# Performance work log

Hardware: AMD Instinct MI355X
Metric: run time of the kernel (lower is better)

The kernel has to match this reference:

```python
import jax, jax.numpy as jnp
import numpy as np

EPS_IN = 1e-5   # InstanceNorm eps
EPS_L1 = 1e-12  # F.normalize eps


def conv1x1(x, w, b):
    # x: [B,C,H,W], w: [O,C], b: [O]
    return jnp.einsum('bchw,oc->bohw', x, w) + b[None, :, None, None]


def conv3x3_reflect(x, w, b):
    xp = jnp.pad(x, ((0, 0), (0, 0), (1, 1), (1, 1)), mode='reflect')
    y = jax.lax.conv_general_dilated(xp, w, (1, 1), 'VALID',
                                     dimension_numbers=('NCHW', 'OIHW', 'NCHW'))
    return y + b[None, :, None, None]


def instance_norm(x):
    mu = x.mean(axis=(2, 3), keepdims=True)
    var = x.var(axis=(2, 3), keepdims=True)  # biased, matches torch InstanceNorm
    return (x - mu) * jax.lax.rsqrt(var + EPS_IN)


def res_block(x, w1, b1, w2, b2):
    h = jax.nn.relu(instance_norm(conv3x3_reflect(x, w1, b1)))
    h = instance_norm(conv3x3_reflect(h, w2, b2))
    return x + h


def _nearest_idx(out_size, in_size):
    # torch F.interpolate(mode='nearest'): src = floor(dst * in/out)
    return (np.arange(out_size) * in_size) // out_size


def forward(x, mask, g_w, g_b, theta_w, theta_b, phi_w, phi_b, W_w, W_b,
            res_w1, res_b1, res_w2, res_b2):
    B, C, H, Wd = x.shape
    N = H * Wd
    g_x = conv1x1(x, g_w, g_b).reshape(B, -1, N).transpose(0, 2, 1)      # [B,N,Ci]
    theta_x = conv1x1(x, theta_w, theta_b).reshape(B, -1, N).transpose(0, 2, 1)
    phi_x = conv1x1(x, phi_w, phi_b).reshape(B, -1, N)                   # [B,Ci,N]
    f = jnp.einsum('bnc,bcm->bnm', theta_x, phi_x)  # temperature = 1.0
    f_div_C = jax.nn.softmax(f, axis=2)
    # mask pipeline
    m = jax.image.resize(mask, (B, 1, H, Wd), method='linear')  # bilinear, half-pixel (align_corners=False)
    m = jnp.where(m > 0, 1.0, m)
    m = 1.0 - m
    hi = _nearest_idx(H, mask.shape[2])
    wi = _nearest_idx(Wd, mask.shape[3])
    tmp = (1.0 - mask)[:, :, hi][:, :, :, wi]  # nearest upsample of (1-mask)
    m = m * tmp                                 # [B,1,H,W]
    f_div_C = f_div_C * m.reshape(B, 1, N)      # broadcast instead of N^2 repeat
    # re_norm=True: L1 renormalize along keys
    f_div_C = f_div_C / jnp.maximum(jnp.sum(jnp.abs(f_div_C), axis=2, keepdims=True), EPS_L1)
    y = jnp.einsum('bnm,bmc->bnc', f_div_C, g_x)             # [B,N,Ci]
    y = y.transpose(0, 2, 1).reshape(B, -1, H, Wd)
    W_y = conv1x1(y, W_w, W_b)
    for i in range(3):
        W_y = res_block(W_y, res_w1[i], res_b1[i], res_w2[i], res_b2[i])
    z = m * x + (1.0 - m) * W_y
    return z


def setup_inputs() -> dict:
    key = jax.random.key(0)
    ks = jax.random.split(key, 16)
    B, C, H, W = 4, 256, 64, 64
    x = jax.random.normal(ks[0], (B, C, H, W), dtype=jnp.float32)
    mask = (jax.random.uniform(ks[1], (B, 1, 32, 32)) < 0.5).astype(jnp.float32)
    s = 0.02
    d = {
        'x': x, 'mask': mask,
        'g_w': jax.random.normal(ks[2], (C, C), jnp.float32) * s,
        'g_b': jnp.zeros((C,), jnp.float32),
        'theta_w': jax.random.normal(ks[3], (C, C), jnp.float32) * s,
        'theta_b': jnp.zeros((C,), jnp.float32),
        'phi_w': jax.random.normal(ks[4], (C, C), jnp.float32) * s,
        'phi_b': jnp.zeros((C,), jnp.float32),
        'W_w': jax.random.normal(ks[5], (C, C), jnp.float32) * s,
        'W_b': jnp.zeros((C,), jnp.float32),
        'res_w1': jax.random.normal(ks[6], (3, C, C, 3, 3), jnp.float32) * s,
        'res_b1': jnp.zeros((3, C), jnp.float32),
        'res_w2': jax.random.normal(ks[7], (3, C, C, 3, 3), jnp.float32) * s,
        'res_b2': jnp.zeros((3, C), jnp.float32),
    }
    return d


def reference(x, mask, g_w, g_b, theta_w, theta_b, phi_w, phi_b, W_w, W_b,
              res_w1, res_b1, res_w2, res_b2):
    return forward(x, mask, g_w, g_b, theta_w, theta_b, phi_w, phi_b, W_w, W_b,
                   res_w1, res_b1, res_w2, res_b2)
```

## Files before the change

kernel.cpp:

```cpp
#include <hip/hip_runtime.h>

#define BB   4
#define CC   256
#define NPIX 4096
#define PB   1048576
#define NTOT 16384

typedef __attribute__((ext_vector_type(8))) short bf16x8;
typedef __attribute__((ext_vector_type(4))) float f32x4;
typedef __attribute__((ext_vector_type(4))) unsigned short u16x4;

__device__ __forceinline__ unsigned short f2b(float f) {
  union { float f; unsigned u; } v; v.f = f;
  unsigned r = v.u + 0x7fffu + ((v.u >> 16) & 1u);
  return (unsigned short)(r >> 16);
}
__device__ __forceinline__ float b2f(unsigned short h) {
  union { unsigned u; float f; } v; v.u = ((unsigned)h) << 16;
  return v.f;
}
__device__ __forceinline__ f32x4 mfma16(bf16x8 a, bf16x8 b, f32x4 c) {
  return __builtin_amdgcn_mfma_f32_16x16x32_bf16(a, b, c, 0, 0, 0);
}
__device__ __forceinline__ void gload_lds16(const unsigned short* g, unsigned short* l) {
  __builtin_amdgcn_global_load_lds(
      (const __attribute__((address_space(1))) unsigned int*)g,
      (__attribute__((address_space(3))) unsigned int*)l, 16, 0, 0);
}
__device__ __forceinline__ int remap_px(int n, int dh, int dw) {
  int h = (n >> 6) + dh;
  int w = (n & 63) + dw;
  h = h < 0 ? 1 : (h > 63 ? 62 : h);
  w = w < 0 ? 1 : (w > 63 ? 62 : w);
  return (h << 6) | w;
}

__global__ void repack_w1x1_k(const float* __restrict__ tw, const float* __restrict__ pw,
                              const float* __restrict__ gw, const float* __restrict__ Ww,
                              unsigned short* __restrict__ dst) {
  int i = blockIdx.x * 256 + threadIdx.x;
  dst[i]           = f2b(tw[i]);
  dst[65536 + i]   = f2b(pw[i]);
  dst[131072 + i]  = f2b(gw[i]);
  dst[196608 + i]  = f2b(Ww[i]);
}

__global__ void repack_bias_k(const float* __restrict__ tb, const float* __restrict__ pb,
                              const float* __restrict__ gb, const float* __restrict__ Wb,
                              float* __restrict__ bias) {
  int i = blockIdx.x * 256 + threadIdx.x;
  float v;
  if (i < 256) v = tb[i];
  else if (i < 512) v = pb[i - 256];
  else if (i < 768) v = gb[i - 512];
  else v = Wb[i - 768];
  bias[i] = v;
}

__global__ void repack_res_k(const float* __restrict__ w1, const float* __restrict__ w2,
                             unsigned short* __restrict__ wk) {
  int idx = blockIdx.x * 256 + threadIdx.x;
  if (idx >= 1769472) return;
  int t = idx % 9;
  int rest = idx / 9;
  int c = rest & 255;
  int o = (rest >> 8) & 255;
  int i = rest >> 16;
  size_t d = (size_t)t * 65536 + o * 256 + c;
  wk[(size_t)(2 * i)     * 589824 + d] = f2b(w1[idx]);
  wk[(size_t)(2 * i + 1) * 589824 + d] = f2b(w2[idx]);
}

__global__ void prep_mask_k(const float* __restrict__ mask, float* __restrict__ m) {
  int idx = blockIdx.x * 256 + threadIdx.x;
  if (idx >= BB * NPIX) return;
  int b = idx >> 12, n = idx & 4095;
  int h = n >> 6, w = n & 63;
  const float* M = mask + b * 1024;
  float sh = 0.5f * h - 0.25f, sw = 0.5f * w - 0.25f;
  int h0 = (int)floorf(sh), w0 = (int)floorf(sw);
  float th = sh - h0, tw = sw - w0;
  int h0c = min(max(h0, 0), 31), h1c = min(max(h0 + 1, 0), 31);
  int w0c = min(max(w0, 0), 31), w1c = min(max(w0 + 1, 0), 31);
  float v = (1.f - th) * ((1.f - tw) * M[h0c * 32 + w0c] + tw * M[h0c * 32 + w1c])
          +        th  * ((1.f - tw) * M[h1c * 32 + w0c] + tw * M[h1c * 32 + w1c]);
  float inv = v > 0.f ? 0.f : 1.f;
  float tmp = 1.f - M[(h >> 1) * 32 + (w >> 1)];
  m[idx] = inv * tmp;
}

__global__ void mask_scan_k(const float* __restrict__ mbuf, int* __restrict__ ci,
                            int* __restrict__ kcount) {
  int b = blockIdx.x;
  int tid = threadIdx.x;
  __shared__ int sc[256];
  const float* mb = mbuf + b * 4096;
  int n0 = tid * 16, cnt = 0;
  float mv[16];
  #pragma unroll
  for (int i = 0; i < 16; ++i) { mv[i] = mb[n0 + i]; cnt += mv[i] > 0.f ? 1 : 0; }
  sc[tid] = cnt;
  __syncthreads();
  for (int off = 1; off < 256; off <<= 1) {
    int v = sc[tid];
    int u = tid >= off ? sc[tid - off] : 0;
    __syncthreads();
    sc[tid] = v + u;
    __syncthreads();
  }
  int base = sc[tid] - cnt;
  int* cib = ci + b * 4096;
  #pragma unroll
  for (int i = 0; i < 16; ++i)
    if (mv[i] > 0.f) cib[base++] = n0 + i;
  if (tid == 255) kcount[b] = sc[255];
}

__global__ void gather_phi_k(const unsigned short* __restrict__ phb, const int* __restrict__ ci,
                             const int* __restrict__ kcount, unsigned short* __restrict__ phic) {
  int b = blockIdx.y;
  int Kb = kcount[b];
  int pad = (Kb + 63) & ~63;
  int j = blockIdx.x * 8 + (threadIdx.x >> 5);
  int cl = threadIdx.x & 31;
  if (j >= pad) return;
  bf16x8 v;
  if (j < Kb) {
    v = *(const bf16x8*)(phb + (size_t)b * PB + (size_t)ci[b * 4096 + j] * 256 + cl * 8);
  } else {
    for (int t = 0; t < 8; ++t) v[t] = 0;
  }
  *(bf16x8*)(phic + (size_t)b * PB + (size_t)j * 256 + cl * 8) = v;
}

__global__ void gather_g_k(const unsigned short* __restrict__ gbuf, const int* __restrict__ ci,
                           const int* __restrict__ kcount, unsigned short* __restrict__ gc) {
  int b = blockIdx.z;
  int Kb = kcount[b];
  int pad = (Kb + 63) & ~63;
  int c = blockIdx.y;
  int j = blockIdx.x * 256 + threadIdx.x;
  if (j >= pad) return;
  unsigned short v = 0;
  if (j < Kb) v = gbuf[(size_t)c * NTOT + b * 4096 + ci[b * 4096 + j]];
  gc[(size_t)c * NTOT + b * 4096 + j] = v;
}

__global__ void transpose_x_k(const float* __restrict__ x, unsigned short* __restrict__ xT) {
  __shared__ float T[64][65];
  int b = blockIdx.z;
  int n0 = blockIdx.x * 64, c0 = blockIdx.y * 64;
  int tx = threadIdx.x, ty = threadIdx.y;
  const float* xb = x + (size_t)b * PB;
  #pragma unroll
  for (int i = 0; i < 16; ++i) {
    int cl = ty + i * 4;
    T[cl][tx] = xb[(size_t)(c0 + cl) * NPIX + n0 + tx];
  }
  __syncthreads();
  unsigned short* ob = xT + (size_t)b * PB;
  #pragma unroll
  for (int i = 0; i < 16; ++i) {
    int nl = ty + i * 4;
    ob[(size_t)(n0 + nl) * CC + c0 + tx] = f2b(T[tx][nl]);
  }
}

template <int EPI, int TAPS>
__launch_bounds__(128, 2)
__global__ void gemm_w(const unsigned short* __restrict__ A,
                       const unsigned short* __restrict__ Bact,
                       const float* __restrict__ bias,
                       float* __restrict__ outF,
                       unsigned short* __restrict__ o0,
                       unsigned short* __restrict__ o1,
                       unsigned short* __restrict__ o2) {
  int m0 = blockIdx.y * 128;
  int bxs = (blockIdx.x & 7) * 32 + (blockIdx.x >> 3);
  int n0 = bxs * 64;
  int tid = threadIdx.x, lane = tid & 63, wid = tid >> 6;
  int r16 = lane & 15, g4 = lane >> 4;
  __shared__ __align__(16) unsigned short As[2 * 8192];
  __shared__ __align__(16) unsigned short Bs[2 * 4096];
  f32x4 acc[4][4] = {};
  int sr[8], sc[8];
  #pragma unroll
  for (int q = 0; q < 8; ++q) {
    sr[q] = (tid >> 3) + q * 16;
    sc[q] = (((tid * 16) & 127) ^ ((sr[q] & 7) << 4)) >> 1;
  }
  int q7 = r16 & 7;
  int ra[4], rbv[4];
  #pragma unroll
  for (int i = 0; i < 4; ++i) ra[i] = (wid * 64 + i * 16 + r16) * 128;
  #pragma unroll
  for (int j = 0; j < 4; ++j) rbv[j] = (j * 16 + r16) * 128;

  const int nsteps = TAPS * 4;

#define STAGE(st_, bs_) do {                                                      \
    int tap_ = (st_) >> 2, k0_ = ((st_) & 3) * 64;                                \
    const unsigned short* At_ = A + tap_ * 65536;                                 \
    _Pragma("unroll")                                                             \
    for (int q = 0; q < 8; ++q)                                                   \
      gload_lds16(At_ + (size_t)(m0 + sr[q]) * 256 + k0_ + sc[q],                 \
                  &As[(bs_) * 8192 + tid * 8 + q * 1024]);                        \
    _Pragma("unroll")                                                             \
    for (int q = 0; q < 4; ++q) {                                                 \
      int n_ = n0 + sr[q];                                                        \
      int bsrc_ = n_;                                                             \
      if (TAPS == 9) bsrc_ = (n_ & ~4095) | remap_px(n_ & 4095, tap_ / 3 - 1, tap_ % 3 - 1); \
      gload_lds16(Bact + (size_t)bsrc_ * 256 + k0_ + sc[q],                       \
                  &Bs[(bs_) * 4096 + tid * 8 + q * 1024]);                        \
    }                                                                             \
  } while (0)

#define COMPUTE(bs_) do {                                                         \
    _Pragma("unroll")                                                             \
    for (int kk = 0; kk < 2; ++kk) {                                              \
      bf16x8 af_[4], bf_[4];                                                      \
      _Pragma("unroll")                                                           \
      for (int i = 0; i < 4; ++i)                                                 \
        af_[i] = *(const bf16x8*)((const char*)As + (bs_) * 16384 + ra[i] +       \
                                  (((kk * 4 + g4) ^ q7) << 4));                   \
      _Pragma("unroll")                                                           \
      for (int j = 0; j < 4; ++j)                                                 \
        bf_[j] = *(const bf16x8*)((const char*)Bs + (bs_) * 8192 + rbv[j] +       \
                                  (((kk * 4 + g4) ^ q7) << 4));                   \
      _Pragma("unroll")                                                           \
      for (int i = 0; i < 4; ++i)                                                 \
        _Pragma("unroll")                                                         \
        for (int j = 0; j < 4; ++j)                                               \
          acc[i][j] = mfma16(af_[i], bf_[j], acc[i][j]);                          \
    }                                                                             \
  } while (0)

  STAGE(0, 0);
  for (int st = 0; st < nsteps; ++st) {
    __syncthreads();
    if (st + 1 < nsteps) STAGE(st + 1, (st + 1) & 1);
    COMPUTE(st & 1);
  }
#undef STAGE
#undef COMPUTE

  #pragma unroll
  for (int i = 0; i < 4; ++i) {
    int row = m0 + wid * 64 + i * 16 + g4 * 4;
    #pragma unroll
    for (int j = 0; j < 4; ++j) {
      int n = n0 + j * 16 + r16;
      f32x4 v = acc[i][j];
      if constexpr (EPI == 0) {
        int sec = row >> 8;
        int ch = row & 255;
        if (sec < 2) {
          u16x4 pk;
          #pragma unroll
          for (int r = 0; r < 4; ++r) pk[r] = f2b(v[r] + bias[row + r]);
          *(u16x4*)((sec ? o1 : o0) + (size_t)n * 256 + ch) = pk;
        } else {
          #pragma unroll
          for (int r = 0; r < 4; ++r)
            o2[(size_t)(ch + r) * NTOT + n] = f2b(v[r] + bias[row + r]);
        }
      } else if constexpr (EPI == 1) {
        u16x4 pk;
        #pragma unroll
        for (int r = 0; r < 4; ++r) pk[r] = f2b(v[r]);
        *(u16x4*)(o0 + (size_t)n * 256 + row) = pk;
      } else {
        #pragma unroll
        for (int r = 0; r < 4; ++r) v[r] += bias[row + r];
        *(f32x4*)(outF + (size_t)n * 256 + row) = v;
        u16x4 pk;
        #pragma unroll
        for (int r = 0; r < 4; ++r) pk[r] = f2b(v[r]);
        *(u16x4*)(o0 + (size_t)n * 256 + row) = pk;
      }
    }
  }
}

__launch_bounds__(512, 2)
__global__ void attn_k(const unsigned short* __restrict__ theta,
                       const unsigned short* __restrict__ phic,
                       const unsigned short* __restrict__ gc,
                       const int* __restrict__ kcount,
                       float* __restrict__ Op0,
                       float* __restrict__ Op1,
                       float2* __restrict__ ml2) {
  int f = blockIdx.x;
  int b = (f & 7) >> 1;
  int s = f & 1;
  int q0 = (f >> 3) * 128;
  int tid = threadIdx.x, lane = tid & 63, wid = tid >> 6;
  int r16 = lane & 15, g4 = lane >> 4;
  const unsigned short* th = theta + (size_t)b * PB;
  const unsigned short* phb = phic + (size_t)b * PB;

  int Kb = kcount[b];
  int nt = (Kb + 63) >> 6;
  int h = (nt + 1) >> 1;
  int t0 = s * h, t1 = min(nt, t0 + h);

  __shared__ __align__(16) unsigned short Kt[2][16384];
  __shared__ __align__(16) unsigned short Vt[2][16384];
  __shared__ __align__(16) unsigned short Plds[8][16][72];

  int qrow = q0 + wid * 16 + r16;
  bf16x8 aq[8];
  #pragma unroll
  for (int ks = 0; ks < 8; ++ks)
    aq[ks] = *(const bf16x8*)(th + (size_t)qrow * CC + ks * 32 + 8 * g4);

  f32x4 O[16];
  #pragma unroll
  for (int cf = 0; cf < 16; ++cf) { O[cf][0] = 0.f; O[cf][1] = 0.f; O[cf][2] = 0.f; O[cf][3] = 0.f; }
  float mrow[4] = {-1e30f, -1e30f, -1e30f, -1e30f};
  float lrow[4] = {0.f, 0.f, 0.f, 0.f};

  bf16x8 kst[4], vst[4];
  if (t0 < t1) {
    int k0g = t0 * 64;
    #pragma unroll
    for (int i = 0; i < 4; ++i) {
      int slot = wid * 4 + i;
      kst[i] = *(const bf16x8*)(phb + (size_t)(k0g + lane) * CC + slot * 8);
      vst[i] = *(const bf16x8*)(gc + (size_t)(i * 64 + lane) * NTOT + b * 4096 + k0g + wid * 8);
    }
    #pragma unroll
    for (int i = 0; i < 4; ++i) {
      int slot = wid * 4 + i;
      *(bf16x8*)&Kt[0][slot * 512 + lane * 8] = kst[i];
      *(bf16x8*)&Vt[0][wid * 2048 + i * 512 + lane * 8] = vst[i];
    }
  }
  __syncthreads();

  #pragma unroll 1
  for (int t = t0; t < t1; ++t) {
    int p = (t - t0) & 1;
    if (t + 1 < t1) {
      int k0g = (t + 1) * 64;
      #pragma unroll
      for (int i = 0; i < 4; ++i) {
        int slot = wid * 4 + i;
        kst[i] = *(const bf16x8*)(phb + (size_t)(k0g + lane) * CC + slot * 8);
        vst[i] = *(const bf16x8*)(gc + (size_t)(i * 64 + lane) * NTOT + b * 4096 + k0g + wid * 8);
      }
    }
    f32x4 S[4];
    #pragma unroll
    for (int ff = 0; ff < 4; ++ff) { S[ff][0] = 0.f; S[ff][1] = 0.f; S[ff][2] = 0.f; S[ff][3] = 0.f; }
    #pragma unroll
    for (int ks = 0; ks < 8; ++ks) {
      #pragma unroll
      for (int ff = 0; ff < 4; ++ff) {
        bf16x8 bk = *(const bf16x8*)&Kt[p][(ks * 4 + g4) * 512 + (ff * 16 + r16) * 8];
        S[ff] = mfma16(aq[ks], bk, S[ff]);
      }
    }
    bool mk[4];
    #pragma unroll
    for (int ff = 0; ff < 4; ++ff) mk[ff] = (t * 64 + ff * 16 + r16) < Kb;
    float scr[4];
    #pragma unroll
    for (int r = 0; r < 4; ++r) {
      float v = -1e30f;
      #pragma unroll
      for (int ff = 0; ff < 4; ++ff) v = fmaxf(v, mk[ff] ? S[ff][r] : -1e30f);
      v = fmaxf(v, __shfl_xor(v, 1));
      v = fmaxf(v, __shfl_xor(v, 2));
      v = fmaxf(v, __shfl_xor(v, 4));
      v = fmaxf(v, __shfl_xor(v, 8));
      float nm = fmaxf(mrow[r], v);
      scr[r] = __expf(mrow[r] - nm);
      mrow[r] = nm;
      lrow[r] *= scr[r];
    }
    float ps[4][4];
    float rsum[4] = {0.f, 0.f, 0.f, 0.f};
    #pragma unroll
    for (int ff = 0; ff < 4; ++ff)
      #pragma unroll
      for (int r = 0; r < 4; ++r) {
        float pp = mk[ff] ? __expf(S[ff][r] - mrow[r]) : 0.f;
        ps[ff][r] = pp;
        rsum[r] += pp;
      }
    #pragma unroll
    for (int r = 0; r < 4; ++r) {
      float sm = rsum[r];
      sm += __shfl_xor(sm, 1);
      sm += __shfl_xor(sm, 2);
      sm += __shfl_xor(sm, 4);
      sm += __shfl_xor(sm, 8);
      lrow[r] += sm;
    }
    #pragma unroll
    for (int cf = 0; cf < 16; ++cf) {
      O[cf][0] *= scr[0]; O[cf][1] *= scr[1]; O[cf][2] *= scr[2]; O[cf][3] *= scr[3];
    }
    #pragma unroll
    for (int ff = 0; ff < 4; ++ff)
      #pragma unroll
      for (int r = 0; r < 4; ++r)
        Plds[wid][g4 * 4 + r][ff * 16 + r16] = f2b(ps[ff][r]);
    #pragma unroll
    for (int ks2 = 0; ks2 < 2; ++ks2) {
      bf16x8 ap = *(const bf16x8*)&Plds[wid][r16][ks2 * 32 + 8 * g4];
      #pragma unroll
      for (int cf = 0; cf < 16; ++cf) {
        bf16x8 bv = *(const bf16x8*)&Vt[p][(ks2 * 4 + g4) * 2048 + (cf * 16 + r16) * 8];
        O[cf] = mfma16(ap, bv, O[cf]);
      }
    }
    if (t + 1 < t1) {
      #pragma unroll
      for (int i = 0; i < 4; ++i) {
        int slot = wid * 4 + i;
        *(bf16x8*)&Kt[p ^ 1][slot * 512 + lane * 8] = kst[i];
        *(bf16x8*)&Vt[p ^ 1][wid * 2048 + i * 512 + lane * 8] = vst[i];
      }
    }
    __syncthreads();
  }

  float* Opb = (s ? Op1 : Op0) + (size_t)b * NPIX * CC;
  #pragma unroll
  for (int cf = 0; cf < 16; ++cf)
    #pragma unroll
    for (int r = 0; r < 4; ++r)
      Opb[(size_t)(q0 + wid * 16 + g4 * 4 + r) * CC + cf * 16 + r16] = O[cf][r];
  if (r16 == 0) {
    #pragma unroll
    for (int r = 0; r < 4; ++r)
      ml2[(size_t)(s * BB + b) * NPIX + q0 + wid * 16 + g4 * 4 + r] =
          make_float2(mrow[r], lrow[r]);
  }
}

__global__ void attn_combine_k(const float* __restrict__ Op0, const float* __restrict__ Op1,
                               const float2* __restrict__ ml2, unsigned short* __restrict__ y) {
  size_t e = ((size_t)blockIdx.x * 256 + threadIdx.x) * 8;
  int bn = (int)(e >> 8);
  float2 a = ml2[bn];
  float2 c = ml2[16384 + bn];
  float M = fmaxf(a.x, c.x);
  float e0 = __expf(a.x - M), e1 = __expf(c.x - M);
  float L = a.y * e0 + c.y * e1;
  float sc = L > 1e-30f ? 1.f / L : 0.f;
  e0 *= sc; e1 *= sc;
  f32x4 p0 = *(const f32x4*)&Op0[e];
  f32x4 p1 = *(const f32x4*)&Op0[e + 4];
  f32x4 q0 = *(const f32x4*)&Op1[e];
  f32x4 q1 = *(const f32x4*)&Op1[e + 4];
  bf16x8 r;
  #pragma unroll
  for (int j = 0; j < 4; ++j) {
    r[j]     = (short)f2b(p0[j] * e0 + q0[j] * e1);
    r[4 + j] = (short)f2b(p1[j] * e0 + q1[j] * e1);
  }
  *(bf16x8*)&y[e] = r;
}

__global__ void in_stats_k(const unsigned short* __restrict__ v,
                           float* __restrict__ psum, float* __restrict__ psumsq) {
  int p = blockIdx.x;
  int b = blockIdx.y;
  int tid = threadIdx.x;
  int cg = (tid & 31) * 8;
  int rsub = tid >> 5;
  const unsigned short* base = v + (size_t)b * PB + (size_t)p * 128 * CC;
  float s[8] = {}, s2[8] = {};
  for (int it = 0; it < 16; ++it) {
    int row = rsub + it * 8;
    bf16x8 x = *(const bf16x8*)(base + (size_t)row * CC + cg);
    #pragma unroll
    for (int j = 0; j < 8; ++j) {
      float f = b2f((unsigned short)x[j]);
      s[j] += f; s2[j] += f * f;
    }
  }
  __shared__ float redS[8][256];
  __shared__ float redQ[8][256];
  #pragma unroll
  for (int j = 0; j < 8; ++j) { redS[rsub][cg + j] = s[j]; redQ[rsub][cg + j] = s2[j]; }
  __syncthreads();
  float a = 0.f, q = 0.f;
  #pragma unroll
  for (int r = 0; r < 8; ++r) { a += redS[r][tid]; q += redQ[r][tid]; }
  int o = (p * BB + b) * CC + tid;
  psum[o] = a; psumsq[o] = q;
}

__global__ void in_finalize_k(const float* __restrict__ psum, const float* __restrict__ psumsq,
                              float* __restrict__ mu, float* __restrict__ rs) {
  int bc = blockIdx.x * 256 + threadIdx.x;
  int b = bc >> 8, c = bc & 255;
  float s = 0.f, s2 = 0.f;
  for (int p = 0; p < 32; ++p) {
    s  += psum[(p * BB + b) * CC + c];
    s2 += psumsq[(p * BB + b) * CC + c];
  }
  float m_ = s * (1.f / 4096.f);
  float var = s2 * (1.f / 4096.f) - m_ * m_;
  var = var > 0.f ? var : 0.f;
  mu[bc] = m_;
  rs[bc] = rsqrtf(var + 1e-5f);
}

__global__ void normrelu_k(const unsigned short* __restrict__ src,
                           const float* __restrict__ mu, const float* __restrict__ rs,
                           unsigned short* __restrict__ dst) {
  size_t idx = (size_t)blockIdx.x * 256 + threadIdx.x;
  size_t e = idx * 8;
  if (e >= (size_t)BB * PB) return;
  int c = (int)(e & 255);
  int b = (int)(e >> 20);
  const float* mup = mu + b * 256 + c;
  const float* rsp = rs + b * 256 + c;
  bf16x8 v = *(const bf16x8*)(src + e);
  bf16x8 ov;
  #pragma unroll
  for (int j = 0; j < 8; ++j) {
    float f = (b2f((unsigned short)v[j]) - mup[j]) * rsp[j];
    ov[j] = (short)f2b(f > 0.f ? f : 0.f);
  }
  *(bf16x8*)(dst + e) = ov;
}

__global__ void resupdate_k(const unsigned short* __restrict__ c2,
                            const float* __restrict__ mu, const float* __restrict__ rs,
                            float* __restrict__ r, unsigned short* __restrict__ rb) {
  size_t idx = (size_t)blockIdx.x * 256 + threadIdx.x;
  size_t e = idx * 8;
  if (e >= (size_t)BB * PB) return;
  int c = (int)(e & 255);
  int b = (int)(e >> 20);
  const float* mup = mu + b * 256 + c;
  const float* rsp = rs + b * 256 + c;
  bf16x8 v = *(const bf16x8*)(c2 + e);
  bf16x8 ov;
  #pragma unroll
  for (int j = 0; j < 8; ++j) {
    float f = r[e + j] + (b2f((unsigned short)v[j]) - mup[j]) * rsp[j];
    r[e + j] = f;
    ov[j] = (short)f2b(f);
  }
  *(bf16x8*)(rb + e) = ov;
}

__global__ void final_blend_k(const float* __restrict__ x, const float* __restrict__ r,
                              const float* __restrict__ m, float* __restrict__ out) {
  __shared__ float T[64][65];
  int b = blockIdx.z;
  int n0 = blockIdx.x * 64, c0 = blockIdx.y * 64;
  int tx = threadIdx.x, ty = threadIdx.y;
  #pragma unroll
  for (int i = 0; i < 16; ++i) {
    int nl = ty + i * 4;
    T[nl][tx] = r[(size_t)b * PB + (size_t)(n0 + nl) * CC + c0 + tx];
  }
  __syncthreads();
  #pragma unroll
  for (int i = 0; i < 16; ++i) {
    int cl = ty + i * 4;
    int cg = c0 + cl, ng = n0 + tx;
    float mv = m[b * NPIX + ng];
    float xv = x[(size_t)b * PB + (size_t)cg * NPIX + ng];
    out[(size_t)b * PB + (size_t)cg * NPIX + ng] = mv * xv + (1.f - mv) * T[tx][cl];
  }
}

#define OFF_M    0UL
#define OFF_XT   65536UL
#define OFF_TH   8454144UL
#define OFF_PH   16842752UL
#define OFF_G    25231360UL
#define OFF_R    33619968UL
#define OFF_W1   50397184UL
#define OFF_WK   50921472UL
#define OFF_MU   57999360UL
#define OFF_RS   58003456UL
#define OFF_PS   58007552UL
#define OFF_PS2  58138624UL
#define OFF_OP1  58269696UL
#define OFF_ML   75046912UL
#define OFF_CI   75309056UL
#define OFF_KC   75374592UL
#define OFF_BIAS 75374848UL

extern "C" void kernel_launch(void* const* d_in, const int* in_sizes, int n_in,
                              void* d_out, int out_size, void* d_ws, size_t ws_size,
                              hipStream_t stream) {
  const float* x       = (const float*)d_in[0];
  const float* maskp   = (const float*)d_in[1];
  const float* g_w     = (const float*)d_in[2];
  const float* g_b     = (const float*)d_in[3];
  const float* theta_w = (const float*)d_in[4];
  const float* theta_b = (const float*)d_in[5];
  const float* phi_w   = (const float*)d_in[6];
  const float* phi_b   = (const float*)d_in[7];
  const float* W_w     = (const float*)d_in[8];
  const float* W_b     = (const float*)d_in[9];
  const float* res_w1  = (const float*)d_in[10];
  const float* res_w2  = (const float*)d_in[12];
  float* out = (float*)d_out;
  char* ws = (char*)d_ws;

  float*          mbuf = (float*)(ws + OFF_M);
  unsigned short* xT   = (unsigned short*)(ws + OFF_XT);
  unsigned short* phic = (unsigned short*)(ws + OFF_XT);
  unsigned short* ybuf = (unsigned short*)(ws + OFF_XT);
  unsigned short* thb  = (unsigned short*)(ws + OFF_TH);
  unsigned short* cbuf = (unsigned short*)(ws + OFF_TH);
  unsigned short* phb  = (unsigned short*)(ws + OFF_PH);
  unsigned short* gc   = (unsigned short*)(ws + OFF_PH);
  unsigned short* hbuf = (unsigned short*)(ws + OFF_PH);
  unsigned short* gbuf = (unsigned short*)(ws + OFF_G);
  unsigned short* rb   = (unsigned short*)(ws + OFF_G);
  float*          rbuf = (float*)(ws + OFF_R);
  float*          op0  = (float*)(ws + OFF_R);
  float*          op1  = (float*)(ws + OFF_OP1);
  float2*         ml2  = (float2*)(ws + OFF_ML);
  int*            ci   = (int*)(ws + OFF_CI);
  int*            kc   = (int*)(ws + OFF_KC);
  float*          biasS= (float*)(ws + OFF_BIAS);
  unsigned short* thw  = (unsigned short*)(ws + OFF_W1);
  unsigned short* Www  = (unsigned short*)(ws + OFF_W1 + 393216);
  unsigned short* wkres= (unsigned short*)(ws + OFF_WK);
  float*          mu   = (float*)(ws + OFF_MU);
  float*          rs   = (float*)(ws + OFF_RS);
  float*          psum = (float*)(ws + OFF_PS);
  float*          psq  = (float*)(ws + OFF_PS2);

  repack_w1x1_k<<<256, 256, 0, stream>>>(theta_w, phi_w, g_w, W_w, thw);
  repack_res_k<<<6912, 256, 0, stream>>>(res_w1, res_w2, wkres);
  repack_bias_k<<<4, 256, 0, stream>>>(theta_b, phi_b, g_b, W_b, biasS);
  prep_mask_k<<<64, 256, 0, stream>>>(maskp, mbuf);
  transpose_x_k<<<dim3(64, 4, 4), dim3(64, 4), 0, stream>>>(x, xT);

  gemm_w<0, 1><<<dim3(256, 6), 128, 0, stream>>>(thw, xT, biasS, nullptr, thb, phb, gbuf);

  mask_scan_k<<<4, 256, 0, stream>>>(mbuf, ci, kc);
  gather_phi_k<<<dim3(512, 4), 256, 0, stream>>>(phb, ci, kc, phic);
  gather_g_k<<<dim3(16, 256, 4), 256, 0, stream>>>(gbuf, ci, kc, gc);

  attn_k<<<256, 512, 0, stream>>>(thb, phic, gc, kc, op0, op1, ml2);
  attn_combine_k<<<2048, 256, 0, stream>>>(op0, op1, ml2, ybuf);

  gemm_w<2, 1><<<dim3(256, 2), 128, 0, stream>>>(Www, ybuf, biasS + 768, rbuf, rb, nullptr, nullptr);

  for (int i = 0; i < 3; ++i) {
    gemm_w<1, 9><<<dim3(256, 2), 128, 0, stream>>>(
        wkres + (size_t)(2 * i) * 589824, rb, nullptr, nullptr, cbuf, nullptr, nullptr);
    in_stats_k<<<dim3(32, 4), 256, 0, stream>>>(cbuf, psum, psq);
    in_finalize_k<<<4, 256, 0, stream>>>(psum, psq, mu, rs);
    normrelu_k<<<2048, 256, 0, stream>>>(cbuf, mu, rs, hbuf);
    gemm_w<1, 9><<<dim3(256, 2), 128, 0, stream>>>(
        wkres + (size_t)(2 * i + 1) * 589824, hbuf, nullptr, nullptr, cbuf, nullptr, nullptr);
    in_stats_k<<<dim3(32, 4), 256, 0, stream>>>(cbuf, psum, psq);
    in_finalize_k<<<4, 256, 0, stream>>>(psum, psq, mu, rs);
    resupdate_k<<<2048, 256, 0, stream>>>(cbuf, mu, rs, rbuf, rb);
  }

  final_blend_k<<<dim3(64, 4, 4), dim3(64, 4), 0, stream>>>(x, rbuf, mbuf, out);
}
```

Before: 589.6 us.

## Enlarge GEMM tiles to 128x128 and split-K the 3x3 convs with fused stats combine

New measurement: 499.8 us. 1.18x faster.

```diff
diff --git a/kernel.cpp b/kernel.cpp
--- a/kernel.cpp
+++ b/kernel.cpp
@@ -166,8 +166,8 @@
   }
 }
 
-template <int EPI, int TAPS>
-__launch_bounds__(128, 2)
+template <int EPI, int TAPS, int KSPLIT>
+__launch_bounds__(256, 2)
 __global__ void gemm_w(const unsigned short* __restrict__ A,
                        const unsigned short* __restrict__ Bact,
                        const float* __restrict__ bias,
@@ -176,42 +176,42 @@
                        unsigned short* __restrict__ o1,
                        unsigned short* __restrict__ o2) {
   int m0 = blockIdx.y * 128;
-  int bxs = (blockIdx.x & 7) * 32 + (blockIdx.x >> 3);
-  int n0 = bxs * 64;
+  int bxs = (blockIdx.x & 7) * 16 + (blockIdx.x >> 3);
+  int n0 = bxs * 128;
   int tid = threadIdx.x, lane = tid & 63, wid = tid >> 6;
+  int wm = wid >> 1, wn = wid & 1;
   int r16 = lane & 15, g4 = lane >> 4;
   __shared__ __align__(16) unsigned short As[2 * 8192];
-  __shared__ __align__(16) unsigned short Bs[2 * 4096];
+  __shared__ __align__(16) unsigned short Bs[2 * 8192];
   f32x4 acc[4][4] = {};
-  int sr[8], sc[8];
-  #pragma unroll
-  for (int q = 0; q < 8; ++q) {
-    sr[q] = (tid >> 3) + q * 16;
-    sc[q] = (((tid * 16) & 127) ^ ((sr[q] & 7) << 4)) >> 1;
-  }
+  int r0 = tid >> 3;
+  int scol = ((((tid * 16) & 127) ^ ((r0 & 7) << 4)) >> 1);
   int q7 = r16 & 7;
   int ra[4], rbv[4];
   #pragma unroll
-  for (int i = 0; i < 4; ++i) ra[i] = (wid * 64 + i * 16 + r16) * 128;
-  #pragma unroll
-  for (int j = 0; j < 4; ++j) rbv[j] = (j * 16 + r16) * 128;
+  for (int i = 0; i < 4; ++i) ra[i] = (wm * 64 + i * 16 + r16) * 128;
+  #pragma unroll
+  for (int j = 0; j < 4; ++j) rbv[j] = (wn * 64 + j * 16 + r16) * 128;
 
   const int nsteps = TAPS * 4;
+  const int span = nsteps / KSPLIT;
+  const int s0 = (KSPLIT > 1 ? blockIdx.z : 0) * span;
+  const int s1 = s0 + span;
 
 #define STAGE(st_, bs_) do {                                                      \
     int tap_ = (st_) >> 2, k0_ = ((st_) & 3) * 64;                                \
     const unsigned short* At_ = A + tap_ * 65536;                                 \
     _Pragma("unroll")                                                             \
-    for (int q = 0; q < 8; ++q)                                                   \
-      gload_lds16(At_ + (size_t)(m0 + sr[q]) * 256 + k0_ + sc[q],                 \
-                  &As[(bs_) * 8192 + tid * 8 + q * 1024]);                        \
+    for (int q = 0; q < 4; ++q)                                                   \
+      gload_lds16(At_ + (size_t)(m0 + r0 + q * 32) * 256 + k0_ + scol,            \
+                  &As[(bs_) * 8192 + tid * 8 + q * 2048]);                        \
     _Pragma("unroll")                                                             \
     for (int q = 0; q < 4; ++q) {                                                 \
-      int n_ = n0 + sr[q];                                                        \
+      int n_ = n0 + r0 + q * 32;                                                  \
       int bsrc_ = n_;                                                             \
       if (TAPS == 9) bsrc_ = (n_ & ~4095) | remap_px(n_ & 4095, tap_ / 3 - 1, tap_ % 3 - 1); \
-      gload_lds16(Bact + (size_t)bsrc_ * 256 + k0_ + sc[q],                       \
-                  &Bs[(bs_) * 4096 + tid * 8 + q * 1024]);                        \
+      gload_lds16(Bact + (size_t)bsrc_ * 256 + k0_ + scol,                        \
+                  &Bs[(bs_) * 8192 + tid * 8 + q * 2048]);                        \
     }                                                                             \
   } while (0)
 
@@ -225,7 +225,7 @@
                                   (((kk * 4 + g4) ^ q7) << 4));                   \
       _Pragma("unroll")                                                           \
       for (int j = 0; j < 4; ++j)                                                 \
-        bf_[j] = *(const bf16x8*)((const char*)Bs + (bs_) * 8192 + rbv[j] +       \
+        bf_[j] = *(const bf16x8*)((const char*)Bs + (bs_) * 16384 + rbv[j] +      \
                                   (((kk * 4 + g4) ^ q7) << 4));                   \
       _Pragma("unroll")                                                           \
       for (int i = 0; i < 4; ++i)                                                 \
@@ -235,21 +235,21 @@
     }                                                                             \
   } while (0)
 
-  STAGE(0, 0);
-  for (int st = 0; st < nsteps; ++st) {
+  STAGE(s0, 0);
+  for (int st = s0; st < s1; ++st) {
     __syncthreads();
-    if (st + 1 < nsteps) STAGE(st + 1, (st + 1) & 1);
-    COMPUTE(st & 1);
+    if (st + 1 < s1) STAGE(st + 1, (st + 1 - s0) & 1);
+    COMPUTE((st - s0) & 1);
   }
 #undef STAGE
 #undef COMPUTE
 
   #pragma unroll
   for (int i = 0; i < 4; ++i) {
-    int row = m0 + wid * 64 + i * 16 + g4 * 4;
+    int row = m0 + wm * 64 + i * 16 + g4 * 4;
     #pragma unroll
     for (int j = 0; j < 4; ++j) {
-      int n = n0 + j * 16 + r16;
+      int n = n0 + wn * 64 + j * 16 + r16;
       f32x4 v = acc[i][j];
       if constexpr (EPI == 0) {
         int sec = row >> 8;
@@ -269,7 +269,7 @@
         #pragma unroll
         for (int r = 0; r < 4; ++r) pk[r] = f2b(v[r]);
         *(u16x4*)(o0 + (size_t)n * 256 + row) = pk;
-      } else {
+      } else if constexpr (EPI == 2) {
         #pragma unroll
         for (int r = 0; r < 4; ++r) v[r] += bias[row + r];
         *(f32x4*)(outF + (size_t)n * 256 + row) = v;
@@ -277,9 +277,54 @@
         #pragma unroll
         for (int r = 0; r < 4; ++r) pk[r] = f2b(v[r]);
         *(u16x4*)(o0 + (size_t)n * 256 + row) = pk;
+      } else {
+        float* dst = blockIdx.z ? (float*)o0 : outF;
+        *(f32x4*)&dst[(size_t)n * 256 + row] = v;
       }
     }
   }
+}
+
+__global__ void combine_stats_k(const float* __restrict__ p0, const float* __restrict__ p1,
+                                unsigned short* __restrict__ cb,
+                                float* __restrict__ psum, float* __restrict__ psq) {
+  int p = blockIdx.x;
+  int b = blockIdx.y;
+  int tid = threadIdx.x;
+  int cg = (tid & 31) * 8;
+  int rsub = tid >> 5;
+  size_t base = ((size_t)b * 4096 + p * 128) * 256;
+  float s[8] = {}, s2[8] = {};
+  for (int it = 0; it < 16; ++it) {
+    int row = rsub + it * 8;
+    size_t e = base + (size_t)row * 256 + cg;
+    f32x4 a0 = *(const f32x4*)&p0[e];
+    f32x4 a1 = *(const f32x4*)&p0[e + 4];
+    f32x4 c0 = *(const f32x4*)&p1[e];
+    f32x4 c1 = *(const f32x4*)&p1[e + 4];
+    bf16x8 ov;
+    #pragma unroll
+    for (int j = 0; j < 4; ++j) {
+      float f = a0[j] + c0[j];
+      ov[j] = (short)f2b(f); s[j] += f; s2[j] += f * f;
+    }
+    #pragma unroll
+    for (int j = 0; j < 4; ++j) {
+      float f = a1[j] + c1[j];
+      ov[4 + j] = (short)f2b(f); s[4 + j] += f; s2[4 + j] += f * f;
+    }
+    *(bf16x8*)&cb[e] = ov;
+  }
+  __shared__ float redS[8][256];
+  __shared__ float redQ[8][256];
+  #pragma unroll
+  for (int j = 0; j < 8; ++j) { redS[rsub][cg + j] = s[j]; redQ[rsub][cg + j] = s2[j]; }
+  __syncthreads();
+  float a = 0.f, q = 0.f;
+  #pragma unroll
+  for (int r = 0; r < 8; ++r) { a += redS[r][tid]; q += redQ[r][tid]; }
+  int o = (p * BB + b) * CC + tid;
+  psum[o] = a; psq[o] = q;
 }
 
 __launch_bounds__(512, 2)
@@ -463,36 +508,6 @@
     r[4 + j] = (short)f2b(p1[j] * e0 + q1[j] * e1);
   }
   *(bf16x8*)&y[e] = r;
-}
-
-__global__ void in_stats_k(const unsigned short* __restrict__ v,
-                           float* __restrict__ psum, float* __restrict__ psumsq) {
-  int p = blockIdx.x;
-  int b = blockIdx.y;
-  int tid = threadIdx.x;
-  int cg = (tid & 31) * 8;
-  int rsub = tid >> 5;
-  const unsigned short* base = v + (size_t)b * PB + (size_t)p * 128 * CC;
-  float s[8] = {}, s2[8] = {};
-  for (int it = 0; it < 16; ++it) {
-    int row = rsub + it * 8;
-    bf16x8 x = *(const bf16x8*)(base + (size_t)row * CC + cg);
-    #pragma unroll
-    for (int j = 0; j < 8; ++j) {
-      float f = b2f((unsigned short)x[j]);
-      s[j] += f; s2[j] += f * f;
-    }
-  }
-  __shared__ float redS[8][256];
-  __shared__ float redQ[8][256];
-  #pragma unroll
-  for (int j = 0; j < 8; ++j) { redS[rsub][cg + j] = s[j]; redQ[rsub][cg + j] = s2[j]; }
-  __syncthreads();
-  float a = 0.f, q = 0.f;
-  #pragma unroll
-  for (int r = 0; r < 8; ++r) { a += redS[r][tid]; q += redQ[r][tid]; }
-  int o = (p * BB + b) * CC + tid;
-  psum[o] = a; psumsq[o] = q;
 }
 
 __global__ void in_finalize_k(const float* __restrict__ psum, const float* __restrict__ psumsq,
@@ -622,8 +637,10 @@
   unsigned short* gbuf = (unsigned short*)(ws + OFF_G);
   unsigned short* rb   = (unsigned short*)(ws + OFF_G);
   float*          rbuf = (float*)(ws + OFF_R);
-  float*          op0  = (float*)(ws + OFF_R);
-  float*          op1  = (float*)(ws + OFF_OP1);
+  float*          aop0 = (float*)(ws + OFF_R);
+  float*          aop1 = (float*)(ws + OFF_OP1);
+  float*          cp0  = (float*)(ws + OFF_OP1);
+  float*          cp1  = out;
   float2*         ml2  = (float2*)(ws + OFF_ML);
   int*            ci   = (int*)(ws + OFF_CI);
   int*            kc   = (int*)(ws + OFF_KC);
@@ -642,26 +659,29 @@
   prep_mask_k<<<64, 256, 0, stream>>>(maskp, mbuf);
   transpose_x_k<<<dim3(64, 4, 4), dim3(64, 4), 0, stream>>>(x, xT);
 
-  gemm_w<0, 1><<<dim3(256, 6), 128, 0, stream>>>(thw, xT, biasS, nullptr, thb, phb, gbuf);
+  gemm_w<0, 1, 1><<<dim3(128, 6), 256, 0, stream>>>(thw, xT, biasS, nullptr, thb, phb, gbuf);
 
   mask_scan_k<<<4, 256, 0, stream>>>(mbuf, ci, kc);
   gather_phi_k<<<dim3(512, 4), 256, 0, stream>>>(phb, ci, kc, phic);
   gather_g_k<<<dim3(16, 256, 4), 256, 0, stream>>>(gbuf, ci, kc, gc);
 
-  attn_k<<<256, 512, 0, stream>>>(thb, phic, gc, kc, op0, op1, ml2);
-  attn_combine_k<<<2048, 256, 0, stream>>>(op0, op1, ml2, ybuf);
-
-  gemm_w<2, 1><<<dim3(256, 2), 128, 0, stream>>>(Www, ybuf, biasS + 768, rbuf, rb, nullptr, nullptr);
+  attn_k<<<256, 512, 0, stream>>>(thb, phic, gc, kc, aop0, aop1, ml2);
+  attn_combine_k<<<2048, 256, 0, stream>>>(aop0, aop1, ml2, ybuf);
+
+  gemm_w<2, 1, 1><<<dim3(128, 2), 256, 0, stream>>>(Www, ybuf, biasS + 768, rbuf, rb,
+                                                    nullptr, nullptr);
 
   for (int i = 0; i < 3; ++i) {
-    gemm_w<1, 9><<<dim3(256, 2), 128, 0, stream>>>(
-        wkres + (size_t)(2 * i) * 589824, rb, nullptr, nullptr, cbuf, nullptr, nullptr);
-    in_stats_k<<<dim3(32, 4), 256, 0, stream>>>(cbuf, psum, psq);
+    gemm_w<3, 9, 2><<<dim3(128, 2, 2), 256, 0, stream>>>(
+        wkres + (size_t)(2 * i) * 589824, rb, nullptr, cp0,
+        (unsigned short*)cp1, nullptr, nullptr);
+    combine_stats_k<<<dim3(32, 4), 256, 0, stream>>>(cp0, cp1, cbuf, psum, psq);
     in_finalize_k<<<4, 256, 0, stream>>>(psum, psq, mu, rs);
     normrelu_k<<<2048, 256, 0, stream>>>(cbuf, mu, rs, hbuf);
-    gemm_w<1, 9><<<dim3(256, 2), 128, 0, stream>>>(
-        wkres + (size_t)(2 * i + 1) * 589824, hbuf, nullptr, nullptr, cbuf, nullptr, nullptr);
-    in_stats_k<<<dim3(32, 4), 256, 0, stream>>>(cbuf, psum, psq);
+    gemm_w<3, 9, 2><<<dim3(128, 2, 2), 256, 0, stream>>>(
+        wkres + (size_t)(2 * i + 1) * 589824, hbuf, nullptr, cp0,
+        (unsigned short*)cp1, nullptr, nullptr);
+    combine_stats_k<<<dim3(32, 4), 256, 0, stream>>>(cp0, cp1, cbuf, psum, psq);
     in_finalize_k<<<4, 256, 0, stream>>>(psum, psq, mu, rs);
     resupdate_k<<<2048, 256, 0, stream>>>(cbuf, mu, rs, rbuf, rb);
   }
```
